# Kernel optimization log

Hardware: AMD Instinct MI355X
Metric: run time of the kernel (lower is better)

## Reference

```python
import jax, jax.numpy as jnp
import numpy as np

ALPHA = 0.2  # LeakyReLU negative slope
NEG_INF = -9e15


def setup_inputs() -> dict:
    key = jax.random.key(0)
    k_h, k_adj, k_W, k_a = jax.random.split(key, 4)
    B, N, Din, Dout = 8, 1024, 256, 256
    h = jax.random.normal(k_h, (B, N, Din), dtype=jnp.float32)
    adj = jax.random.randint(k_adj, (B, N, N), 0, 2, dtype=jnp.int32)
    # nn.Linear weight [out, in], xavier-uniform-ish init for a
    W = jax.random.normal(k_W, (Dout, Din), dtype=jnp.float32) * (1.0 / np.sqrt(Din))
    lim = np.float32(1.414 * np.sqrt(6.0 / (2 * Dout + 1)))
    a = jax.random.uniform(k_a, (2 * Dout, 1), dtype=jnp.float32, minval=-lim, maxval=lim)
    return {"h": h, "adj": adj, "W": W, "a": a}


def reference(h, adj, W, a):
    # Wh: [B, N, F]
    Wh = jnp.einsum('bnd,fd->bnf', h, W)
    F_ = Wh.shape[-1]
    # Decompose concat-then-matmul: e_ij = leakyrelu(Wh_i @ a1 + Wh_j @ a2)
    a1 = a[:F_, 0]   # [F]
    a2 = a[F_:, 0]   # [F]
    src = Wh @ a1    # [B, N]  score contribution of row node i
    dst = Wh @ a2    # [B, N]  score contribution of col node j
    e = src[:, :, None] + dst[:, None, :]          # [B, N, N]
    e = jnp.where(e > 0, e, ALPHA * e)             # LeakyReLU
    e = jnp.where(adj > 0, e, NEG_INF)             # mask non-edges
    attention = jax.nn.softmax(e, axis=-1)         # [B, N, N]
    # dropout p=0.0 -> identity in eval/train
    h_prime = jnp.einsum('bij,bjf->bif', attention, Wh)
    return h_prime
```

## Files before the change

kernel.cpp:

```cpp
#include <hip/hip_runtime.h>
#include <hip/hip_bf16.h>
#include <cstdint>

#define ALPHA 0.2f

typedef __bf16 bf16_t;
typedef __bf16 bf16x8 __attribute__((ext_vector_type(8)));
typedef float f32x16 __attribute__((ext_vector_type(16)));

__global__ __launch_bounds__(256) void k_pre(
    const float* __restrict__ h, const float* __restrict__ W, const float* __restrict__ a,
    const int* __restrict__ adj, bf16_t* __restrict__ WhT,
    float* __restrict__ srcE, float* __restrict__ srcF,
    float* __restrict__ dstE, float* __restrict__ dstF,
    unsigned long long* __restrict__ mask_ws)
{
  __shared__ __align__(16) char smem[64 * 72 * 2 * sizeof(bf16_t)];
  const int bx = blockIdx.x;
  const int t = threadIdx.x;

  if (bx < 512) {
    bf16_t* WS = (bf16_t*)smem;
    bf16_t* HS = WS + 64 * 72;
    const int b  = bx & 7;
    const int jt = (bx >> 3) & 15;
    const int ft = bx >> 7;
    const int j0 = jt * 64, f0 = ft * 64;
    const int w = t >> 6, lane = t & 63;
    const int mrow = lane & 31, half = lane >> 5;
    const int fsub = (w & 1) * 32, jsub = (w >> 1) * 32;

    const int lr = t >> 2;
    const int lc = (t & 3) * 16;
    const float* wp = W + ((size_t)(f0 + lr)) * 256 + lc;
    const float* hp = h + ((size_t)(b * 1024 + j0 + lr)) * 256 + lc;

    f32x16 acc;
#pragma unroll
    for (int r = 0; r < 16; r++) acc[r] = 0.f;

    for (int s = 0; s < 4; s++) {
      if (s) __syncthreads();
      {
        float4 w0 = *(const float4*)(wp + s * 64);
        float4 w1 = *(const float4*)(wp + s * 64 + 4);
        float4 w2 = *(const float4*)(wp + s * 64 + 8);
        float4 w3 = *(const float4*)(wp + s * 64 + 12);
        bf16x8 va, vb;
        va[0] = (bf16_t)w0.x; va[1] = (bf16_t)w0.y; va[2] = (bf16_t)w0.z; va[3] = (bf16_t)w0.w;
        va[4] = (bf16_t)w1.x; va[5] = (bf16_t)w1.y; va[6] = (bf16_t)w1.z; va[7] = (bf16_t)w1.w;
        vb[0] = (bf16_t)w2.x; vb[1] = (bf16_t)w2.y; vb[2] = (bf16_t)w2.z; vb[3] = (bf16_t)w2.w;
        vb[4] = (bf16_t)w3.x; vb[5] = (bf16_t)w3.y; vb[6] = (bf16_t)w3.z; vb[7] = (bf16_t)w3.w;
        *(bf16x8*)&WS[lr * 72 + lc] = va;
        *(bf16x8*)&WS[lr * 72 + lc + 8] = vb;
        float4 h0 = *(const float4*)(hp + s * 64);
        float4 h1 = *(const float4*)(hp + s * 64 + 4);
        float4 h2 = *(const float4*)(hp + s * 64 + 8);
        float4 h3 = *(const float4*)(hp + s * 64 + 12);
        bf16x8 vc, vd;
        vc[0] = (bf16_t)h0.x; vc[1] = (bf16_t)h0.y; vc[2] = (bf16_t)h0.z; vc[3] = (bf16_t)h0.w;
        vc[4] = (bf16_t)h1.x; vc[5] = (bf16_t)h1.y; vc[6] = (bf16_t)h1.z; vc[7] = (bf16_t)h1.w;
        vd[0] = (bf16_t)h2.x; vd[1] = (bf16_t)h2.y; vd[2] = (bf16_t)h2.z; vd[3] = (bf16_t)h2.w;
        vd[4] = (bf16_t)h3.x; vd[5] = (bf16_t)h3.y; vd[6] = (bf16_t)h3.z; vd[7] = (bf16_t)h3.w;
        *(bf16x8*)&HS[lr * 72 + lc] = vc;
        *(bf16x8*)&HS[lr * 72 + lc + 8] = vd;
      }
      __syncthreads();
#pragma unroll
      for (int ks = 0; ks < 4; ks++) {
        bf16x8 af = *(const bf16x8*)&WS[(fsub + mrow) * 72 + ks * 16 + half * 8];
        bf16x8 bf = *(const bf16x8*)&HS[(jsub + mrow) * 72 + ks * 16 + half * 8];
        acc = __builtin_amdgcn_mfma_f32_32x32x16_bf16(af, bf, acc, 0, 0, 0);
      }
    }

    const int jcol = j0 + jsub + mrow;
#pragma unroll
    for (int r = 0; r < 16; r++) {
      int frow = fsub + (r & 3) + 8 * (r >> 2) + 4 * half;
      WhT[(((size_t)(b * 256 + f0 + frow)) << 10) + jcol] = (bf16_t)acc[r];
    }
  } else {
    float* uS = (float*)smem;
    const int p  = bx - 512;
    const int m0 = p * 16;
    {
      float s1a = 0.f, s1b = 0.f, s2a = 0.f, s2b = 0.f;
#pragma unroll 4
      for (int f = 0; f < 256; f += 2) {
        float w0 = W[f * 256 + t];
        float w1 = W[(f + 1) * 256 + t];
        s1a = fmaf(w0, a[f], s1a);       s1b = fmaf(w1, a[f + 1], s1b);
        s2a = fmaf(w0, a[256 + f], s2a); s2b = fmaf(w1, a[256 + f + 1], s2b);
      }
      uS[t] = s1a + s1b; uS[256 + t] = s2a + s2b;
    }
    __syncthreads();
    {
      const int n = t >> 4, c = t & 15;
      const int m = m0 + n;
      const float* hp = h + (size_t)m * 256 + c * 16;
      float s1 = 0.f, s2 = 0.f;
#pragma unroll
      for (int i = 0; i < 4; i++) {
        float4 v = *(const float4*)(hp + i * 4);
        const float* u1p = &uS[c * 16 + i * 4];
        const float* u2p = &uS[256 + c * 16 + i * 4];
        s1 = fmaf(v.x, u1p[0], s1); s1 = fmaf(v.y, u1p[1], s1);
        s1 = fmaf(v.z, u1p[2], s1); s1 = fmaf(v.w, u1p[3], s1);
        s2 = fmaf(v.x, u2p[0], s2); s2 = fmaf(v.y, u2p[1], s2);
        s2 = fmaf(v.z, u2p[2], s2); s2 = fmaf(v.w, u2p[3], s2);
      }
#pragma unroll
      for (int off = 8; off; off >>= 1) {
        s1 += __shfl_down(s1, off, 16);
        s2 += __shfl_down(s2, off, 16);
      }
      if (c == 0) {
        srcE[m] = __expf(s1); srcF[m] = __expf(ALPHA * s1);
        dstE[m] = __expf(s2); dstF[m] = __expf(ALPHA * s2);
      }
    }
    {
      const int wv = t >> 6, lane = t & 63;
#pragma unroll 4
      for (int r = 0; r < 16; r++) {
        const size_t row = (size_t)(m0 + r);
        const int* ap = adj + (row << 10) + t;
        unsigned long long b0 = __ballot(ap[0] > 0);
        unsigned long long b1 = __ballot(ap[256] > 0);
        unsigned long long b2 = __ballot(ap[512] > 0);
        unsigned long long b3 = __ballot(ap[768] > 0);
        if (lane == 0) {
          unsigned long long* mp = mask_ws + row * 16 + wv;
          mp[0] = b0; mp[4] = b1; mp[8] = b2; mp[12] = b3;
        }
      }
    }
  }
}

__global__ __launch_bounds__(512) void k_attn(
    const bf16_t* __restrict__ WhT,
    const float* __restrict__ srcEg, const float* __restrict__ srcFg,
    const float* __restrict__ dstEg, const float* __restrict__ dstFg,
    const unsigned long long* __restrict__ mask_ws, float* __restrict__ out)
{
  const int b  = blockIdx.x & 7;
  const int i0 = (blockIdx.x >> 3) << 5;
  const int t  = threadIdx.x;
  const int w  = t >> 6;
  const int lane = t & 63;
  const int mrow = lane & 31, half = lane >> 5;
  const int ip = t & 31;
  const int g  = t >> 5;

  __shared__ float dstE_s[1024], dstF_s[1024];
  __shared__ unsigned long long maskS[32 * 16];
  __shared__ bf16_t P[2][32 * 264];
  __shared__ float rsS[512];
  __shared__ float rowRcp[32];

  if (t < 256) {
    float4 v = *(const float4*)(dstEg + (b << 10) + t * 4);
    *(float4*)&dstE_s[t * 4] = v;
  } else {
    float4 v = *(const float4*)(dstFg + (b << 10) + (t - 256) * 4);
    *(float4*)&dstF_s[(t - 256) * 4] = v;
  }
  maskS[t] = mask_ws[((size_t)((b << 10) + i0)) * 16 + t];
  const float srcEi = srcEg[(b << 10) + i0 + ip];
  const float srcFi = srcFg[(b << 10) + i0 + ip];
  __syncthreads();

  unsigned long long mw[4];
#pragma unroll
  for (int c = 0; c < 4; c++) mw[c] = maskS[ip * 16 + 4 * c + (g >> 2)];
  const int sh = (g & 3) * 16;

  f32x16 acc;
#pragma unroll
  for (int r = 0; r < 16; r++) acc[r] = 0.f;
  float rsA = 0.f, rsB = 0.f;

  const bf16_t* bp = WhT + (((size_t)(b * 256 + w * 32 + mrow)) << 10);

#pragma unroll
  for (int c = 0; c < 4; c++) {
    bf16_t* Pc = &P[c & 1][0];
    {
      unsigned int m16 = (unsigned int)(mw[c] >> sh);
      float ev[16], fv[16];
      const float* dE = &dstE_s[c * 256 + g * 16];
      const float* dF = &dstF_s[c * 256 + g * 16];
#pragma unroll
      for (int q = 0; q < 4; q++) {
        *(float4*)&ev[q * 4] = *(const float4*)(dE + q * 4);
        *(float4*)&fv[q * 4] = *(const float4*)(dF + q * 4);
      }
      bf16x8 v0, v1;
#pragma unroll
      for (int k = 0; k < 16; k++) {
        float pp = srcEi * ev[k];
        float pn = srcFi * fv[k];
        float pv = (pp > 1.0f) ? pp : pn;
        pv = (m16 & (1u << k)) ? pv : 0.0f;
        if (k & 1) rsB += pv; else rsA += pv;
        bf16_t pb = (bf16_t)pv;
        if (k < 8) v0[k] = pb; else v1[k - 8] = pb;
      }
      *(bf16x8*)&Pc[ip * 264 + g * 16] = v0;
      *(bf16x8*)&Pc[ip * 264 + g * 16 + 8] = v1;
    }
    __syncthreads();

    const bf16_t* bpc = bp + c * 256 + half * 8;
    const bf16_t* prow = Pc + mrow * 264 + half * 8;
#pragma unroll
    for (int idx = 0; idx < 16; idx++) {
      bf16x8 afr = *(const bf16x8*)(prow + idx * 16);
      bf16x8 bfr = *(const bf16x8*)(bpc + idx * 16);
      acc = __builtin_amdgcn_mfma_f32_32x32x16_bf16(afr, bfr, acc, 0, 0, 0);
    }
  }

  rsS[g * 32 + ip] = rsA + rsB;
  __syncthreads();
  if (t < 32) {
    float s = 0.f;
#pragma unroll
    for (int gg = 0; gg < 16; gg++) s += rsS[gg * 32 + t];
    rowRcp[t] = 1.0f / s;
  }
  __syncthreads();

  const int col = w * 32 + mrow;
#pragma unroll
  for (int r = 0; r < 16; r++) {
    int row = (r & 3) + 8 * (r >> 2) + 4 * half;
    out[((size_t)((b << 10) + i0 + row)) * 256 + col] = acc[r] * rowRcp[row];
  }
}

extern "C" void kernel_launch(void* const* d_in, const int* in_sizes, int n_in,
                              void* d_out, int out_size, void* d_ws, size_t ws_size,
                              hipStream_t stream) {
  const float* h   = (const float*)d_in[0];
  const int*   adj = (const int*)d_in[1];
  const float* W   = (const float*)d_in[2];
  const float* a   = (const float*)d_in[3];
  float* out = (float*)d_out;

  char* wsb = (char*)d_ws;
  bf16_t* WhT = (bf16_t*)wsb;
  float* srcE = (float*)(wsb + (4u << 20));
  float* srcF = srcE + 8192;
  float* dstE = srcF + 8192;
  float* dstF = dstE + 8192;
  unsigned long long* mask_ws = (unsigned long long*)(wsb + (4u << 20) + 131072);

  k_pre <<<1024, 256, 0, stream>>>(h, W, a, adj, WhT, srcE, srcF, dstE, dstF, mask_ws);
  k_attn<<<256,  512, 0, stream>>>(WhT, srcE, srcF, dstE, dstF, mask_ws, out);
}
```

Before: 121.3 us.

## Vectorize adjacency mask reads and register-prefetch WhT fragments in attention

```diff
diff --git a/kernel.cpp b/kernel.cpp
--- a/kernel.cpp
+++ b/kernel.cpp
@@ -81,19 +81,22 @@
       WhT[(((size_t)(b * 256 + f0 + frow)) << 10) + jcol] = (bf16_t)acc[r];
     }
   } else {
-    float* uS = (float*)smem;
+    float* aS = (float*)smem;
+    float* uS = aS + 512;
     const int p  = bx - 512;
     const int m0 = p * 16;
-    {
-      float s1a = 0.f, s1b = 0.f, s2a = 0.f, s2b = 0.f;
-#pragma unroll 4
-      for (int f = 0; f < 256; f += 2) {
+    aS[t] = a[t];
+    aS[t + 256] = a[t + 256];
+    __syncthreads();
+    {
+      float s1 = 0.f, s2 = 0.f;
+#pragma unroll 8
+      for (int f = 0; f < 256; f++) {
         float w0 = W[f * 256 + t];
-        float w1 = W[(f + 1) * 256 + t];
-        s1a = fmaf(w0, a[f], s1a);       s1b = fmaf(w1, a[f + 1], s1b);
-        s2a = fmaf(w0, a[256 + f], s2a); s2b = fmaf(w1, a[256 + f + 1], s2b);
-      }
-      uS[t] = s1a + s1b; uS[256 + t] = s2a + s2b;
+        s1 = fmaf(w0, aS[f], s1);
+        s2 = fmaf(w0, aS[256 + f], s2);
+      }
+      uS[t] = s1; uS[256 + t] = s2;
     }
     __syncthreads();
     {
@@ -126,14 +129,14 @@
 #pragma unroll 4
       for (int r = 0; r < 16; r++) {
         const size_t row = (size_t)(m0 + r);
-        const int* ap = adj + (row << 10) + t;
-        unsigned long long b0 = __ballot(ap[0] > 0);
-        unsigned long long b1 = __ballot(ap[256] > 0);
-        unsigned long long b2 = __ballot(ap[512] > 0);
-        unsigned long long b3 = __ballot(ap[768] > 0);
+        const int4 av = *(const int4*)(adj + (row << 10) + 4 * t);
+        unsigned long long b0 = __ballot(av.x > 0);
+        unsigned long long b1 = __ballot(av.y > 0);
+        unsigned long long b2 = __ballot(av.z > 0);
+        unsigned long long b3 = __ballot(av.w > 0);
         if (lane == 0) {
-          unsigned long long* mp = mask_ws + row * 16 + wv;
-          mp[0] = b0; mp[4] = b1; mp[8] = b2; mp[12] = b3;
+          unsigned long long* mp = mask_ws + row * 16 + wv * 4;
+          mp[0] = b0; mp[1] = b1; mp[2] = b2; mp[3] = b3;
         }
       }
     }
@@ -171,25 +174,27 @@
   maskS[t] = mask_ws[((size_t)((b << 10) + i0)) * 16 + t];
   const float srcEi = srcEg[(b << 10) + i0 + ip];
   const float srcFi = srcFg[(b << 10) + i0 + ip];
+
+  const bf16_t* bp = WhT + (((size_t)(b * 256 + w * 32 + mrow)) << 10) + half * 8;
+  bf16x8 bfr[16];
+#pragma unroll
+  for (int idx = 0; idx < 16; idx++) bfr[idx] = *(const bf16x8*)(bp + idx * 16);
+
   __syncthreads();
-
-  unsigned long long mw[4];
-#pragma unroll
-  for (int c = 0; c < 4; c++) mw[c] = maskS[ip * 16 + 4 * c + (g >> 2)];
-  const int sh = (g & 3) * 16;
 
   f32x16 acc;
 #pragma unroll
   for (int r = 0; r < 16; r++) acc[r] = 0.f;
   float rsA = 0.f, rsB = 0.f;
 
-  const bf16_t* bp = WhT + (((size_t)(b * 256 + w * 32 + mrow)) << 10);
-
 #pragma unroll
   for (int c = 0; c < 4; c++) {
     bf16_t* Pc = &P[c & 1][0];
     {
-      unsigned int m16 = (unsigned int)(mw[c] >> sh);
+      unsigned int q0 = (unsigned int)(maskS[ip * 16 + c * 4 + 0] >> (g * 4));
+      unsigned int q1 = (unsigned int)(maskS[ip * 16 + c * 4 + 1] >> (g * 4));
+      unsigned int q2 = (unsigned int)(maskS[ip * 16 + c * 4 + 2] >> (g * 4));
+      unsigned int q3 = (unsigned int)(maskS[ip * 16 + c * 4 + 3] >> (g * 4));
       float ev[16], fv[16];
       const float* dE = &dstE_s[c * 256 + g * 16];
       const float* dF = &dstF_s[c * 256 + g * 16];
@@ -204,7 +209,8 @@
         float pp = srcEi * ev[k];
         float pn = srcFi * fv[k];
         float pv = (pp > 1.0f) ? pp : pn;
-        pv = (m16 & (1u << k)) ? pv : 0.0f;
+        unsigned int sel = ((k & 3) == 0) ? q0 : ((k & 3) == 1) ? q1 : ((k & 3) == 2) ? q2 : q3;
+        pv = ((sel >> (k >> 2)) & 1u) ? pv : 0.0f;
         if (k & 1) rsB += pv; else rsA += pv;
         bf16_t pb = (bf16_t)pv;
         if (k < 8) v0[k] = pb; else v1[k - 8] = pb;
@@ -214,13 +220,15 @@
     }
     __syncthreads();
 
-    const bf16_t* bpc = bp + c * 256 + half * 8;
     const bf16_t* prow = Pc + mrow * 264 + half * 8;
 #pragma unroll
     for (int idx = 0; idx < 16; idx++) {
       bf16x8 afr = *(const bf16x8*)(prow + idx * 16);
-      bf16x8 bfr = *(const bf16x8*)(bpc + idx * 16);
-      acc = __builtin_amdgcn_mfma_f32_32x32x16_bf16(afr, bfr, acc, 0, 0, 0);
+      acc = __builtin_amdgcn_mfma_f32_32x32x16_bf16(afr, bfr[idx], acc, 0, 0, 0);
+    }
+    if (c < 3) {
+#pragma unroll
+      for (int idx = 0; idx < 16; idx++) bfr[idx] = *(const bf16x8*)(bp + (c + 1) * 256 + idx * 16);
     }
   }
 
```

Result: faster. 115.7 us (median of 2 runs) (-4.6%).
